# Performance work log

Measured on AMD Instinct MI355X. Metric: run time of the kernel, lower is better.

The kernel has to match this reference:

```python
import jax, jax.numpy as jnp
import numpy as np

T, N, E, DH = 4, 10000, 160000, 256
BN_EPS = 1e-5


def setup_inputs() -> dict:
    key = jax.random.key(0)
    ks = jax.random.split(key, 6)
    node_data = jax.random.normal(ks[0], (T, N, DH), dtype=jnp.float32)
    edge_index = jax.random.randint(ks[1], (2, E), 0, N)
    edge_weight = jax.random.uniform(ks[2], (T, E), dtype=jnp.float32)
    W1 = jax.random.normal(ks[3], (3 * DH, DH), dtype=jnp.float32) * 0.02
    b1 = jnp.zeros((DH,), dtype=jnp.float32)
    gamma = jnp.ones((DH,), dtype=jnp.float32)
    beta = jnp.zeros((DH,), dtype=jnp.float32)
    return {"node_data": node_data, "edge_weight": edge_weight, "W1": W1,
            "b1": b1, "gamma": gamma, "beta": beta, "edge_index": edge_index}


def reference(node_data, edge_weight, W1, b1, gamma, beta, edge_index):
    # edge_index: [2, E] with row 0 = source j, row 1 = destination i
    # (ew[t, i, j] multiplies node j and accumulates into node i, as in bmm)
    src, dst = edge_index[0], edge_index[1]

    # sparse bmm: sum_j ew[t,i,j] * node_data[t,j,:]  -> [T, N, DH]
    weighted = node_data[:, src, :] * edge_weight[..., None]  # [T, E, DH]
    sum_neighbor = jax.vmap(lambda m: jax.ops.segment_sum(m, dst, num_segments=N))(weighted)

    # Z = torch.sparse.sum(ew, dim=2); Z[Z == 0] = 1
    Z = jax.vmap(lambda w: jax.ops.segment_sum(w, dst, num_segments=N))(edge_weight)
    Z = jnp.where(Z == 0, 1.0, Z)[..., None]  # [T, N, 1]
    avg_neighbor = sum_neighbor / Z

    # prev_state = cat([zeros(1,N,dh), node_data[1:]], dim=0)  (as in source)
    prev_state = jnp.concatenate(
        [jnp.zeros((1, N, DH), node_data.dtype), node_data[1:]], axis=0)

    x = jnp.concatenate([node_data, prev_state, avg_neighbor], axis=2)
    x = x.reshape(T * N, 3 * DH)

    # ReluFCN: Linear(3*dh -> dh) -> BatchNorm1d (batch stats) -> ReLU
    h = x @ W1 + b1  # [T*N, DH]
    mean = h.mean(axis=0)
    var = h.var(axis=0)
    h = (h - mean) * jax.lax.rsqrt(var + BN_EPS) * gamma + beta
    h = jax.nn.relu(h)
    return h.reshape(T, N, DH)
```

## Files before the change

### kernel.cpp

```cpp
#include <hip/hip_runtime.h>

enum { TT = 4, NNODES = 10000, NEDGES = 160000 };

typedef short v8s __attribute__((ext_vector_type(8)));
typedef float v4f __attribute__((ext_vector_type(4)));

static __device__ __forceinline__ float bf2f(unsigned short u) {
    union { unsigned int i; float f; } c;
    c.i = ((unsigned int)u) << 16;
    return c.f;
}
static __device__ __forceinline__ unsigned short f2bf(float f) {
    union { float f; unsigned int i; } c;
    c.f = f;
    return (unsigned short)((c.i + 0x7FFFu + ((c.i >> 16) & 1u)) >> 16);
}
static __device__ __forceinline__ float u2f(unsigned int u) {
    union { unsigned int i; float f; } c;
    c.i = u;
    return c.f;
}
static __device__ __forceinline__ void acc8(float* a, float w, uint4 u) {
    a[0] += w * u2f(u.x << 16);
    a[1] += w * u2f(u.x & 0xffff0000u);
    a[2] += w * u2f(u.y << 16);
    a[3] += w * u2f(u.y & 0xffff0000u);
    a[4] += w * u2f(u.z << 16);
    a[5] += w * u2f(u.z & 0xffff0000u);
    a[6] += w * u2f(u.w << 16);
    a[7] += w * u2f(u.w & 0xffff0000u);
}

__global__ void GraphConvLayer_91061896610587_kernel() {}

__global__ void zero_k(int* p, int n) {
    int i = blockIdx.x * 256 + threadIdx.x;
    if (i < n) p[i] = 0;
}

__global__ void prep_k(const unsigned short* ndu, const void* s0, const void* s1,
                       const void* s2, int* mode, float* gammaf, float* betaf) {
    __shared__ int cnt;
    __shared__ int score[6];
    __shared__ float vals[6][256];
    int d = threadIdx.x;
    if (d == 0) cnt = 0;
    if (d < 6) score[d] = 0;
    __syncthreads();
    int c = 0;
    for (int j = 0; j < 16; ++j) {
        unsigned short u = ndu[d * 16 + j];
        if ((u & 0x7FFF) >= 0x6000) ++c;
    }
    if (c) atomicAdd(&cnt, c);
    const void* ptrs[3];
    ptrs[0] = s0; ptrs[1] = s1; ptrs[2] = s2;
    for (int q = 0; q < 6; ++q) {
        const void* p = ptrs[q % 3];
        float v = (q < 3) ? bf2f(((const unsigned short*)p)[d]) : ((const float*)p)[d];
        vals[q][d] = v;
        float av = fabsf(v);
        if (av > 0.25f && av < 4.0f) atomicAdd(&score[q], 1);
    }
    __syncthreads();
    if (d == 0) *mode = (cnt > 0) ? 0 : 1;
    int best = 0;
    for (int q = 1; q < 6; ++q)
        if (score[q] > score[best]) best = q;
    float g = (score[best] > 0) ? vals[best][d] : 1.0f;
    int interp = (best >= 3) ? 3 : 0;
    int bslot  = ((best % 3) == 2) ? 1 : 2;
    float b = vals[interp + bslot][d];
    if (!(b == b) || fabsf(b) > 100.f) b = 0.f;
    gammaf[d] = g;
    betaf[d]  = b;
}

__global__ void canon_nd(const int* mode, const void* nd_raw, unsigned short* ndc) {
    if (*mode != 0) return;
    int i = blockIdx.x * 256 + threadIdx.x;
    float4 v = ((const float4*)nd_raw)[i];
    ushort4 o;
    o.x = f2bf(v.x); o.y = f2bf(v.y); o.z = f2bf(v.z); o.w = f2bf(v.w);
    ((ushort4*)ndc)[i] = o;
}

__global__ void pack_w(const int* mode, const void* W1, float* w2f,
                       short* wp0, short* wp1) {
    int gid = blockIdx.x * 256 + threadIdx.x;
    int v   = gid >> 17;
    int rem = gid & 131071;
    int k   = rem >> 8;
    int n   = rem & 255;
    int m   = *mode;
    const unsigned short* Wb = (const unsigned short*)W1;
    const float*          Wf = (const float*)W1;
    float val;
    if (k < 256) {
        val = m ? bf2f(Wb[k * 256 + n]) : Wf[k * 256 + n];
        if (v) val += m ? bf2f(Wb[(k + 256) * 256 + n]) : Wf[(k + 256) * 256 + n];
    } else {
        val = m ? bf2f(Wb[(k + 256) * 256 + n]) : Wf[(k + 256) * 256 + n];
    }
    if (w2f) w2f[v * 131072 + k * 256 + n] = val;
    if (wp0) {
        int dst = ((k >> 5) * 256 + n) * 32 + (k & 31);
        (v ? wp1 : wp0)[dst] = (short)f2bf(val);
    }
}

__global__ void hist_k(const int* ei, int* counts) {
    int e = blockIdx.x * 256 + threadIdx.x;
    if (e < NEDGES) atomicAdd(&counts[ei[NEDGES + e]], 1);
}

__global__ void scan_k(const int* counts, int* offsets) {
    __shared__ int part[256];
    __shared__ int excl[257];
    int t = threadIdx.x;
    int b = t * 40, e = b + 40;
    if (e > NNODES) e = NNODES;
    int s = 0;
    for (int i = b; i < e; ++i) s += counts[i];
    part[t] = s;
    __syncthreads();
    if (t == 0) {
        int run = 0;
        for (int i = 0; i < 256; ++i) { excl[i] = run; run += part[i]; }
        excl[256] = run;
    }
    __syncthreads();
    int run = excl[t];
    for (int i = b; i < e; ++i) { offsets[i] = run; run += counts[i]; }
    if (t == 0) offsets[NNODES] = excl[256];
}

__global__ void scat_k(const int* ei, const int* offsets, int* cursors,
                       int* ssrc, int* seid) {
    int e = blockIdx.x * 256 + threadIdx.x;
    if (e >= NEDGES) return;
    int d = ei[NEDGES + e];
    int pos = offsets[d] + atomicAdd(&cursors[d], 1);
    ssrc[pos] = ei[e];
    seid[pos] = e;
}

__global__ void wgath_k(const int* mode, const void* ew_raw, const int* seid,
                        float* wcsr) {
    int i = blockIdx.x * 256 + threadIdx.x;
    int t = i / NEDGES, p = i - t * NEDGES;
    int e = seid[p];
    wcsr[i] = (*mode == 1) ? bf2f(((const unsigned short*)ew_raw)[t * NEDGES + e])
                           : ((const float*)ew_raw)[t * NEDGES + e];
}

__global__ __launch_bounds__(256) void fused_k(
    const int* mode, const void* nd_raw, const unsigned short* ndc,
    const float* wcsr, const int* offsets, const int* ssrc,
    const short* wp0, const short* wp1,
    unsigned short* h16, float* colsumB, float* colsumsqB) {
    __shared__ unsigned short xs[32 * 520];
    const unsigned short* ndb = (*mode == 1) ? (const unsigned short*)nd_raw : ndc;
    int t   = blockIdx.y;
    int rb  = blockIdx.x * 32;
    int tid = threadIdx.x;

    int node = tid >> 3;
    int sub  = tid & 7;
    int dq   = sub * 32;
    int du   = sub * 4;
    int growc = min(rb + node, NNODES - 1);
    const uint4* ndg = (const uint4*)(ndb + (size_t)t * NNODES * 256);

    uint4 c0 = ndg[(size_t)growc * 32 + du + 0];
    uint4 c1 = ndg[(size_t)growc * 32 + du + 1];
    uint4 c2 = ndg[(size_t)growc * 32 + du + 2];
    uint4 c3 = ndg[(size_t)growc * 32 + du + 3];
    *(uint4*)&xs[node * 520 + dq]      = c0;
    *(uint4*)&xs[node * 520 + dq + 8]  = c1;
    *(uint4*)&xs[node * 520 + dq + 16] = c2;
    *(uint4*)&xs[node * 520 + dq + 24] = c3;

    float a1[32];
#pragma unroll
    for (int j = 0; j < 32; ++j) a1[j] = 0.f;
    float Z = 0.f;
    const float* wrow = wcsr + t * NEDGES;
    int b = offsets[growc], e = offsets[growc + 1];
    int p = b;
    for (; p + 2 <= e; p += 2) {
        int s0 = ssrc[p], s1 = ssrc[p + 1];
        float w0 = wrow[p], w1 = wrow[p + 1];
        const uint4* r0 = ndg + (size_t)s0 * 32 + du;
        const uint4* r1 = ndg + (size_t)s1 * 32 + du;
        uint4 A0 = r0[0], A1 = r0[1], A2 = r0[2], A3 = r0[3];
        uint4 B0 = r1[0], B1 = r1[1], B2 = r1[2], B3 = r1[3];
        Z += w0 + w1;
        acc8(a1 + 0,  w0, A0); acc8(a1 + 8,  w0, A1);
        acc8(a1 + 16, w0, A2); acc8(a1 + 24, w0, A3);
        acc8(a1 + 0,  w1, B0); acc8(a1 + 8,  w1, B1);
        acc8(a1 + 16, w1, B2); acc8(a1 + 24, w1, B3);
    }
    for (; p < e; ++p) {
        int s = ssrc[p];
        float w = wrow[p];
        const uint4* r0 = ndg + (size_t)s * 32 + du;
        uint4 A0 = r0[0], A1 = r0[1], A2 = r0[2], A3 = r0[3];
        Z += w;
        acc8(a1 + 0,  w, A0); acc8(a1 + 8,  w, A1);
        acc8(a1 + 16, w, A2); acc8(a1 + 24, w, A3);
    }
    float inv = (Z == 0.f) ? 1.f : (1.f / Z);
#pragma unroll
    for (int j = 0; j < 32; j += 4) {
        ushort4 o;
        o.x = f2bf(a1[j] * inv);
        o.y = f2bf(a1[j + 1] * inv);
        o.z = f2bf(a1[j + 2] * inv);
        o.w = f2bf(a1[j + 3] * inv);
        *(ushort4*)&xs[node * 520 + 256 + dq + j] = o;
    }
    __syncthreads();

    int wave = tid >> 6;
    int lane = tid & 63;
    int lane15 = lane & 15, quad = lane >> 4;
    const v8s* wp8 = (const v8s*)(t ? wp1 : wp0);

    v4f acc[2][4];
    v4f zero = {0.f, 0.f, 0.f, 0.f};
#pragma unroll
    for (int mf = 0; mf < 2; ++mf)
#pragma unroll
        for (int nf = 0; nf < 4; ++nf) acc[mf][nf] = zero;

#pragma unroll
    for (int kc = 0; kc < 16; ++kc) {
        v8s a0 = *(const v8s*)&xs[lane15 * 520 + kc * 32 + quad * 8];
        v8s a1v = *(const v8s*)&xs[(lane15 + 16) * 520 + kc * 32 + quad * 8];
#pragma unroll
        for (int nf = 0; nf < 4; ++nf) {
            int ntg = wave * 4 + nf;
            v8s bf = wp8[(size_t)(kc * 256 + ntg * 16 + lane15) * 4 + quad];
            acc[0][nf] = __builtin_amdgcn_mfma_f32_16x16x32_bf16(a0, bf, acc[0][nf], 0, 0, 0);
            acc[1][nf] = __builtin_amdgcn_mfma_f32_16x16x32_bf16(a1v, bf, acc[1][nf], 0, 0, 0);
        }
    }

    int bucket = blockIdx.x & 63;
#pragma unroll
    for (int nf = 0; nf < 4; ++nf) {
        int col = (wave * 4 + nf) * 16 + lane15;
        float s1 = 0.f, s2 = 0.f;
#pragma unroll
        for (int mf = 0; mf < 2; ++mf) {
            int rbase = rb + mf * 16 + quad * 4;
#pragma unroll
            for (int r = 0; r < 4; ++r) {
                int row = rbase + r;
                if (row < NNODES) {
                    float v = acc[mf][nf][r];
                    h16[(size_t)(t * NNODES + row) * 256 + col] = f2bf(v);
                    s1 += v; s2 += v * v;
                }
            }
        }
        s1 += __shfl_xor(s1, 16, 64); s1 += __shfl_xor(s1, 32, 64);
        s2 += __shfl_xor(s2, 16, 64); s2 += __shfl_xor(s2, 32, 64);
        if (quad == 0) {
            atomicAdd(&colsumB[bucket * 256 + col], s1);
            atomicAdd(&colsumsqB[bucket * 256 + col], s2);
        }
    }
}

__global__ void statsB_k(const float* colsumB, const float* colsumsqB,
                         const float* gammaf, const float* betaf,
                         float* scale, float* shiftv) {
    int d = threadIdx.x;
    float s1 = 0.f, s2 = 0.f;
    for (int b = 0; b < 64; ++b) {
        s1 += colsumB[b * 256 + d];
        s2 += colsumsqB[b * 256 + d];
    }
    float mean = s1 * (1.f / 40000.f);
    float var  = s2 * (1.f / 40000.f) - mean * mean;
    if (var < 0.f) var = 0.f;
    if (!(var < 1e30f) || !(mean == mean)) { scale[d] = 0.f; shiftv[d] = 2.5f; return; }
    float r  = rsqrtf(var + 1e-5f);
    float sc = gammaf[d] * r;
    scale[d]  = sc;
    shiftv[d] = betaf[d] - mean * sc;
}

__global__ void normb_k(const unsigned short* h16, const float* scale,
                        const float* shiftv, float* out) {
    int i = blockIdx.x * 256 + threadIdx.x;
    int c0 = (i & 63) * 4;
    ushort4 h = ((const ushort4*)h16)[i];
    float4 o;
    float v;
    v = bf2f(h.x) * scale[c0 + 0] + shiftv[c0 + 0]; if (!(v == v)) v = 1.f; o.x = v > 0.f ? v : 0.f;
    v = bf2f(h.y) * scale[c0 + 1] + shiftv[c0 + 1]; if (!(v == v)) v = 1.f; o.y = v > 0.f ? v : 0.f;
    v = bf2f(h.z) * scale[c0 + 2] + shiftv[c0 + 2]; if (!(v == v)) v = 1.f; o.z = v > 0.f ? v : 0.f;
    v = bf2f(h.w) * scale[c0 + 3] + shiftv[c0 + 3]; if (!(v == v)) v = 1.f; o.w = v > 0.f ? v : 0.f;
    ((float4*)out)[i] = o;
}

__global__ void aggv_k(const int* mode, const void* nd_raw, const void* ew_raw,
                       const int* offsets, const int* ssrc, const int* seid,
                       unsigned short* avg) {
    int m   = *mode;
    int wid = blockIdx.x * 4 + (threadIdx.x >> 6);
    int t = wid / NNODES, n = wid - t * NNODES;
    int lane = threadIdx.x & 63;
    float a0 = 0.f, a1 = 0.f, a2 = 0.f, a3 = 0.f, Z = 0.f;
    int b = offsets[n], e = offsets[n + 1];
    for (int p = b; p < e; ++p) {
        int s = ssrc[p];
        int ewi = t * NEDGES + seid[p];
        float w = m ? bf2f(((const unsigned short*)ew_raw)[ewi])
                    : ((const float*)ew_raw)[ewi];
        Z += w;
        int vidx = (t * NNODES + s) * 64 + lane;
        if (m) {
            ushort4 v = ((const ushort4*)nd_raw)[vidx];
            a0 += w * bf2f(v.x); a1 += w * bf2f(v.y);
            a2 += w * bf2f(v.z); a3 += w * bf2f(v.w);
        } else {
            float4 v = ((const float4*)nd_raw)[vidx];
            a0 += w * v.x; a1 += w * v.y; a2 += w * v.z; a3 += w * v.w;
        }
    }
    float inv = (Z == 0.f) ? 1.f : (1.f / Z);
    ushort4 o;
    o.x = f2bf(a0 * inv); o.y = f2bf(a1 * inv);
    o.z = f2bf(a2 * inv); o.w = f2bf(a3 * inv);
    ((ushort4*)avg)[(t * NNODES + n) * 64 + lane] = o;
}

__global__ __launch_bounds__(256) void gemmv_k(
    const int* mode, const void* nd_raw, const unsigned short* avg,
    const float* w2f, float* hbuf) {
    __shared__ float xsf[16 * 512];
    int m   = *mode;
    int bt  = blockIdx.x / 625;
    int rb0 = (blockIdx.x - bt * 625) * 16;
    int tid = threadIdx.x;
    for (int j = 0; j < 32; ++j) {
        int idx = tid + j * 256;
        int r = idx >> 9, k = idx & 511;
        int grow = (bt * NNODES + rb0 + r) * 256;
        float val;
        if (k < 256)
            val = m ? bf2f(((const unsigned short*)nd_raw)[grow + k])
                    : ((const float*)nd_raw)[grow + k];
        else
            val = bf2f(avg[grow + (k - 256)]);
        xsf[idx] = val;
    }
    __syncthreads();
    int r0 = (tid >> 6) * 4;
    const float4* w4 = (const float4*)(w2f + (bt ? 131072 : 0));
    float acc[4][4];
#pragma unroll
    for (int r = 0; r < 4; ++r)
#pragma unroll
        for (int c = 0; c < 4; ++c) acc[r][c] = 0.f;
    const float* x0 = &xsf[(r0 + 0) * 512];
    const float* x1 = &xsf[(r0 + 1) * 512];
    const float* x2 = &xsf[(r0 + 2) * 512];
    const float* x3 = &xsf[(r0 + 3) * 512];
#pragma unroll 8
    for (int k = 0; k < 512; ++k) {
        float4 wv = w4[k * 64 + (tid & 63)];
        float a = x0[k], b = x1[k], c = x2[k], d = x3[k];
        acc[0][0] += a * wv.x; acc[0][1] += a * wv.y; acc[0][2] += a * wv.z; acc[0][3] += a * wv.w;
        acc[1][0] += b * wv.x; acc[1][1] += b * wv.y; acc[1][2] += b * wv.z; acc[1][3] += b * wv.w;
        acc[2][0] += c * wv.x; acc[2][1] += c * wv.y; acc[2][2] += c * wv.z; acc[2][3] += c * wv.w;
        acc[3][0] += d * wv.x; acc[3][1] += d * wv.y; acc[3][2] += d * wv.z; acc[3][3] += d * wv.w;
    }
#pragma unroll
    for (int r = 0; r < 4; ++r) {
        int grow = bt * NNODES + rb0 + r0 + r;
        float4 o;
        o.x = acc[r][0]; o.y = acc[r][1]; o.z = acc[r][2]; o.w = acc[r][3];
        ((float4*)hbuf)[grow * 64 + (tid & 63)] = o;
    }
}

__global__ void stats2_k(const float* hbuf, float* colsum, float* colsumsq) {
    int col = threadIdx.x;
    int rb  = blockIdx.x * 250;
    float s1 = 0.f, s2 = 0.f;
    for (int j = 0; j < 250; ++j) {
        float v = hbuf[(size_t)(rb + j) * 256 + col];
        s1 += v; s2 += v * v;
    }
    atomicAdd(&colsum[col], s1);
    atomicAdd(&colsumsq[col], s2);
}

__global__ void stats_k(const float* colsum, const float* colsumsq,
                        const float* gammaf, const float* betaf,
                        float* scale, float* shiftv) {
    int d = threadIdx.x;
    float mean = colsum[d] * (1.f / 40000.f);
    float var  = colsumsq[d] * (1.f / 40000.f) - mean * mean;
    if (var < 0.f) var = 0.f;
    if (!(var < 1e30f) || !(mean == mean)) { scale[d] = 0.f; shiftv[d] = 2.5f; return; }
    float r  = rsqrtf(var + 1e-5f);
    float sc = gammaf[d] * r;
    scale[d]  = sc;
    shiftv[d] = betaf[d] - mean * sc;
}

__global__ void norm_k(float* hbuf, const float* scale, const float* shiftv) {
    int i = blockIdx.x * 256 + threadIdx.x;
    int c0 = (i & 63) * 4;
    float4 h = ((const float4*)hbuf)[i];
    float4 o;
    float v;
    v = h.x * scale[c0 + 0] + shiftv[c0 + 0]; if (!(v == v)) v = 1.f; o.x = v > 0.f ? v : 0.f;
    v = h.y * scale[c0 + 1] + shiftv[c0 + 1]; if (!(v == v)) v = 1.f; o.y = v > 0.f ? v : 0.f;
    v = h.z * scale[c0 + 2] + shiftv[c0 + 2]; if (!(v == v)) v = 1.f; o.z = v > 0.f ? v : 0.f;
    v = h.w * scale[c0 + 3] + shiftv[c0 + 3]; if (!(v == v)) v = 1.f; o.w = v > 0.f ? v : 0.f;
    ((float4*)hbuf)[i] = o;
}

extern "C" void kernel_launch(void* const* d_in, const int* in_sizes, int n_in,
                              void* d_out, int out_size, void* d_ws, size_t ws_size,
                              hipStream_t stream) {
    const void* nd = d_in[0];
    const void* ew = d_in[1];
    const void* W1 = d_in[2];
    const void* p3 = d_in[3];
    const void* p4 = d_in[4];
    const void* p5 = d_in[5];
    const void* ei = d_in[6];
    {
        const void *nd_ = 0, *ew_ = 0, *W1_ = 0, *ei_ = 0, *s_[3] = {0, 0, 0};
        int ns = 0;
        for (int i = 0; i < n_in; ++i) {
            int s = in_sizes[i];
            if      (s == 10240000) nd_ = d_in[i];
            else if (s == 640000)   ew_ = d_in[i];
            else if (s == 196608)   W1_ = d_in[i];
            else if (s == 320000)   ei_ = d_in[i];
            else if (s == 256 && ns < 3) s_[ns++] = d_in[i];
        }
        if (nd_ && ew_ && W1_ && ei_ && ns == 3) {
            nd = nd_; ew = ew_; W1 = W1_; ei = ei_;
            p3 = s_[0]; p4 = s_[1]; p5 = s_[2];
        }
    }
    float* outp = (float*)d_out;
    const unsigned short* ndu = (const unsigned short*)nd;
    const int* eii = (const int*)ei;

    char* ws = (char*)d_ws;

    if (ws_size >= (size_t)45582464) {
        int*   counts    = (int*)(ws + 0);
        int*   cursors   = (int*)(ws + 40960);
        int*   mode      = (int*)(ws + 81920);
        float* scale     = (float*)(ws + 82944);
        float* shiftv    = (float*)(ws + 83968);
        float* gammaf    = (float*)(ws + 84992);
        float* betaf     = (float*)(ws + 86016);
        float* colsumB   = (float*)(ws + 87040);
        float* colsumsqB = (float*)(ws + 152576);
        int*   offsets   = (int*)(ws + 218112);
        int*   ssrc      = (int*)(ws + 258176);
        int*   seid      = (int*)(ws + 898176);
        float* wcsr      = (float*)(ws + 1538176);
        short* wp0       = (short*)(ws + 4098176);
        short* wp1       = (short*)(ws + 4360320);
        unsigned short* ndc = (unsigned short*)(ws + 4622464);
        unsigned short* h16 = (unsigned short*)(ws + 25102464);
        float* noW = 0;

        zero_k<<<213, 256, 0, stream>>>((int*)ws, 54528);
        prep_k<<<1, 256, 0, stream>>>(ndu, p3, p4, p5, mode, gammaf, betaf);
        canon_nd<<<10000, 256, 0, stream>>>(mode, nd, ndc);
        pack_w<<<1024, 256, 0, stream>>>(mode, W1, noW, wp0, wp1);
        hist_k<<<625, 256, 0, stream>>>(eii, counts);
        scan_k<<<1, 256, 0, stream>>>(counts, offsets);
        scat_k<<<625, 256, 0, stream>>>(eii, offsets, cursors, ssrc, seid);
        wgath_k<<<2500, 256, 0, stream>>>(mode, ew, seid, wcsr);
        fused_k<<<dim3(313, 4), 256, 0, stream>>>(mode, nd, ndc, wcsr, offsets, ssrc,
                                                  wp0, wp1, h16, colsumB, colsumsqB);
        statsB_k<<<1, 256, 0, stream>>>(colsumB, colsumsqB, gammaf, betaf, scale, shiftv);
        normb_k<<<10000, 256, 0, stream>>>(h16, scale, shiftv, outp);
    } else {
        int*   counts   = (int*)(ws + 0);
        int*   cursors  = (int*)(ws + 40960);
        float* colsum   = (float*)(ws + 81920);
        float* colsumsq = (float*)(ws + 82944);
        int*   mode     = (int*)(ws + 83968);
        float* scale    = (float*)(ws + 84032);
        float* shiftv   = (float*)(ws + 85056);
        float* gammaf   = (float*)(ws + 86080);
        float* betaf    = (float*)(ws + 87104);
        int*   offsets  = (int*)(ws + 88128);
        int*   ssrc     = (int*)(ws + 128192);
        int*   seid     = (int*)(ws + 768192);
        float* w2f      = (float*)(ws + 1408192);
        unsigned short* avg = (unsigned short*)(ws + 2457600);
        short* nowp = 0;

        zero_k<<<83, 256, 0, stream>>>((int*)ws, 20994);
        prep_k<<<1, 256, 0, stream>>>(ndu, p3, p4, p5, mode, gammaf, betaf);
        pack_w<<<1024, 256, 0, stream>>>(mode, W1, w2f, nowp, nowp);
        hist_k<<<625, 256, 0, stream>>>(eii, counts);
        scan_k<<<1, 256, 0, stream>>>(counts, offsets);
        scat_k<<<625, 256, 0, stream>>>(eii, offsets, cursors, ssrc, seid);
        aggv_k<<<10000, 256, 0, stream>>>(mode, nd, ew, offsets, ssrc, seid, avg);
        gemmv_k<<<2500, 256, 0, stream>>>(mode, nd, avg, w2f, outp);
        stats2_k<<<160, 256, 0, stream>>>(outp, colsum, colsumsq);
        stats_k<<<1, 256, 0, stream>>>(colsum, colsumsq, gammaf, betaf, scale, shiftv);
        norm_k<<<10000, 256, 0, stream>>>(outp, scale, shiftv);
    }
}
```

Measured before the change: 254.6 us.

## Merge prep kernels, remap fused blocks across XCDs, coalesce gathers, use nontemporal I/O

The zeroing and prep kernels become one launch. Bf16 conversion of node data, weight packing and the edge histogram become another. The CSR scatter now also gathers edge weights, which removes the separate wgath pass. Together this cuts the launch count and an extra pass over seid. fused_k switches to a 1D grid that maps each timestep to XCD-aligned block ids for L2 locality. Its per-thread row loads are interleaved (sub, sub+8, ...) so neighbouring lanes read contiguous 16-byte chunks. The h16 write, its read in normb_k and the output store use nontemporal hints, which could hurt if h16 would otherwise stay resident in cache.

```diff
diff --git a/kernel.cpp b/kernel.cpp
--- a/kernel.cpp
+++ b/kernel.cpp
@@ -4,6 +4,7 @@
 
 typedef short v8s __attribute__((ext_vector_type(8)));
 typedef float v4f __attribute__((ext_vector_type(4)));
+typedef unsigned short u16x4 __attribute__((ext_vector_type(4)));
 
 static __device__ __forceinline__ float bf2f(unsigned short u) {
     union { unsigned int i; float f; } c;
@@ -76,13 +77,83 @@
     betaf[d]  = b;
 }
 
-__global__ void canon_nd(const int* mode, const void* nd_raw, unsigned short* ndc) {
-    if (*mode != 0) return;
-    int i = blockIdx.x * 256 + threadIdx.x;
-    float4 v = ((const float4*)nd_raw)[i];
-    ushort4 o;
-    o.x = f2bf(v.x); o.y = f2bf(v.y); o.z = f2bf(v.z); o.w = f2bf(v.w);
-    ((ushort4*)ndc)[i] = o;
+__global__ void zp_k(int* zp, int zn, const unsigned short* ndu, const void* s0,
+                     const void* s1, const void* s2, int* mode, float* gammaf,
+                     float* betaf) {
+    __shared__ int cnt;
+    __shared__ int score[6];
+    __shared__ float vals[6][256];
+    if (blockIdx.x < 213) {
+        int i = blockIdx.x * 256 + threadIdx.x;
+        if (i < zn) zp[i] = 0;
+        return;
+    }
+    int d = threadIdx.x;
+    if (d == 0) cnt = 0;
+    if (d < 6) score[d] = 0;
+    __syncthreads();
+    int c = 0;
+    for (int j = 0; j < 16; ++j) {
+        unsigned short u = ndu[d * 16 + j];
+        if ((u & 0x7FFF) >= 0x6000) ++c;
+    }
+    if (c) atomicAdd(&cnt, c);
+    const void* ptrs[3];
+    ptrs[0] = s0; ptrs[1] = s1; ptrs[2] = s2;
+    for (int q = 0; q < 6; ++q) {
+        const void* p = ptrs[q % 3];
+        float v = (q < 3) ? bf2f(((const unsigned short*)p)[d]) : ((const float*)p)[d];
+        vals[q][d] = v;
+        float av = fabsf(v);
+        if (av > 0.25f && av < 4.0f) atomicAdd(&score[q], 1);
+    }
+    __syncthreads();
+    if (d == 0) *mode = (cnt > 0) ? 0 : 1;
+    int best = 0;
+    for (int q = 1; q < 6; ++q)
+        if (score[q] > score[best]) best = q;
+    float g = (score[best] > 0) ? vals[best][d] : 1.0f;
+    int interp = (best >= 3) ? 3 : 0;
+    int bslot  = ((best % 3) == 2) ? 1 : 2;
+    float b = vals[interp + bslot][d];
+    if (!(b == b) || fabsf(b) > 100.f) b = 0.f;
+    gammaf[d] = g;
+    betaf[d]  = b;
+}
+
+__global__ void cph_k(const int* mode, const void* nd_raw, unsigned short* ndc,
+                      const void* W1, short* wp0, short* wp1,
+                      const int* ei, int* counts) {
+    int bb = blockIdx.x;
+    if (bb < 10000) {
+        if (*mode != 0) return;
+        int i = bb * 256 + threadIdx.x;
+        float4 v = ((const float4*)nd_raw)[i];
+        ushort4 o;
+        o.x = f2bf(v.x); o.y = f2bf(v.y); o.z = f2bf(v.z); o.w = f2bf(v.w);
+        ((ushort4*)ndc)[i] = o;
+    } else if (bb < 11024) {
+        int gid = (bb - 10000) * 256 + threadIdx.x;
+        int v   = gid >> 17;
+        int rem = gid & 131071;
+        int k   = rem >> 8;
+        int n   = rem & 255;
+        int m   = *mode;
+        const unsigned short* Wb = (const unsigned short*)W1;
+        const float*          Wf = (const float*)W1;
+        float val;
+        if (k < 256) {
+            val = m ? bf2f(Wb[k * 256 + n]) : Wf[k * 256 + n];
+            if (v) val += m ? bf2f(Wb[(k + 256) * 256 + n]) : Wf[(k + 256) * 256 + n];
+        } else {
+            val = m ? bf2f(Wb[(k + 256) * 256 + n]) : Wf[(k + 256) * 256 + n];
+        }
+        int dst = ((k >> 5) * 256 + n) * 32 + (k & 31);
+        (v ? wp1 : wp0)[dst] = (short)f2bf(val);
+    } else {
+        int e = (bb - 11024) * 256 + threadIdx.x;
+        if (e < NEDGES) atomicAdd(&counts[ei[NEDGES + e]], 1);
+    }
 }
 
 __global__ void pack_w(const int* mode, const void* W1, float* w2f,
@@ -145,13 +216,22 @@
     seid[pos] = e;
 }
 
-__global__ void wgath_k(const int* mode, const void* ew_raw, const int* seid,
+__global__ void scatw_k(const int* mode, const int* ei, const void* ew_raw,
+                        const int* offsets, int* cursors, int* ssrc, int* seid,
                         float* wcsr) {
-    int i = blockIdx.x * 256 + threadIdx.x;
-    int t = i / NEDGES, p = i - t * NEDGES;
-    int e = seid[p];
-    wcsr[i] = (*mode == 1) ? bf2f(((const unsigned short*)ew_raw)[t * NEDGES + e])
-                           : ((const float*)ew_raw)[t * NEDGES + e];
+    int e = blockIdx.x * 256 + threadIdx.x;
+    if (e >= NEDGES) return;
+    int d = ei[NEDGES + e];
+    int pos = offsets[d] + atomicAdd(&cursors[d], 1);
+    ssrc[pos] = ei[e];
+    seid[pos] = e;
+    int m = *mode;
+#pragma unroll
+    for (int t = 0; t < TT; ++t) {
+        float w = m ? bf2f(((const unsigned short*)ew_raw)[t * NEDGES + e])
+                    : ((const float*)ew_raw)[t * NEDGES + e];
+        wcsr[t * NEDGES + pos] = w;
+    }
 }
 
 __global__ __launch_bounds__(256) void fused_k(
@@ -160,26 +240,29 @@
     const short* wp0, const short* wp1,
     unsigned short* h16, float* colsumB, float* colsumsqB) {
     __shared__ unsigned short xs[32 * 520];
+    int id  = blockIdx.x;
+    int xcd = id & 7;
+    int t   = xcd & 3;
+    int rbi = ((id >> 3) << 1) + (xcd >> 2);
+    if (rbi >= 313) return;
+    int rb  = rbi * 32;
     const unsigned short* ndb = (*mode == 1) ? (const unsigned short*)nd_raw : ndc;
-    int t   = blockIdx.y;
-    int rb  = blockIdx.x * 32;
     int tid = threadIdx.x;
 
     int node = tid >> 3;
     int sub  = tid & 7;
-    int dq   = sub * 32;
-    int du   = sub * 4;
     int growc = min(rb + node, NNODES - 1);
     const uint4* ndg = (const uint4*)(ndb + (size_t)t * NNODES * 256);
-
-    uint4 c0 = ndg[(size_t)growc * 32 + du + 0];
-    uint4 c1 = ndg[(size_t)growc * 32 + du + 1];
-    uint4 c2 = ndg[(size_t)growc * 32 + du + 2];
-    uint4 c3 = ndg[(size_t)growc * 32 + du + 3];
-    *(uint4*)&xs[node * 520 + dq]      = c0;
-    *(uint4*)&xs[node * 520 + dq + 8]  = c1;
-    *(uint4*)&xs[node * 520 + dq + 16] = c2;
-    *(uint4*)&xs[node * 520 + dq + 24] = c3;
+    const uint4* own = ndg + (size_t)growc * 32;
+
+    uint4 c0 = own[sub];
+    uint4 c1 = own[sub + 8];
+    uint4 c2 = own[sub + 16];
+    uint4 c3 = own[sub + 24];
+    *(uint4*)&xs[node * 520 + sub * 8]            = c0;
+    *(uint4*)&xs[node * 520 + (sub + 8) * 8]      = c1;
+    *(uint4*)&xs[node * 520 + (sub + 16) * 8]     = c2;
+    *(uint4*)&xs[node * 520 + (sub + 24) * 8]     = c3;
 
     float a1[32];
 #pragma unroll
@@ -191,10 +274,10 @@
     for (; p + 2 <= e; p += 2) {
         int s0 = ssrc[p], s1 = ssrc[p + 1];
         float w0 = wrow[p], w1 = wrow[p + 1];
-        const uint4* r0 = ndg + (size_t)s0 * 32 + du;
-        const uint4* r1 = ndg + (size_t)s1 * 32 + du;
-        uint4 A0 = r0[0], A1 = r0[1], A2 = r0[2], A3 = r0[3];
-        uint4 B0 = r1[0], B1 = r1[1], B2 = r1[2], B3 = r1[3];
+        const uint4* r0 = ndg + (size_t)s0 * 32;
+        const uint4* r1 = ndg + (size_t)s1 * 32;
+        uint4 A0 = r0[sub], A1 = r0[sub + 8], A2 = r0[sub + 16], A3 = r0[sub + 24];
+        uint4 B0 = r1[sub], B1 = r1[sub + 8], B2 = r1[sub + 16], B3 = r1[sub + 24];
         Z += w0 + w1;
         acc8(a1 + 0,  w0, A0); acc8(a1 + 8,  w0, A1);
         acc8(a1 + 16, w0, A2); acc8(a1 + 24, w0, A3);
@@ -204,21 +287,26 @@
     for (; p < e; ++p) {
         int s = ssrc[p];
         float w = wrow[p];
-        const uint4* r0 = ndg + (size_t)s * 32 + du;
-        uint4 A0 = r0[0], A1 = r0[1], A2 = r0[2], A3 = r0[3];
+        const uint4* r0 = ndg + (size_t)s * 32;
+        uint4 A0 = r0[sub], A1 = r0[sub + 8], A2 = r0[sub + 16], A3 = r0[sub + 24];
         Z += w;
         acc8(a1 + 0,  w, A0); acc8(a1 + 8,  w, A1);
         acc8(a1 + 16, w, A2); acc8(a1 + 24, w, A3);
     }
     float inv = (Z == 0.f) ? 1.f : (1.f / Z);
 #pragma unroll
-    for (int j = 0; j < 32; j += 4) {
-        ushort4 o;
-        o.x = f2bf(a1[j] * inv);
-        o.y = f2bf(a1[j + 1] * inv);
-        o.z = f2bf(a1[j + 2] * inv);
-        o.w = f2bf(a1[j + 3] * inv);
-        *(ushort4*)&xs[node * 520 + 256 + dq + j] = o;
+    for (int j = 0; j < 4; ++j) {
+        ushort4 lo, hi;
+        lo.x = f2bf(a1[j * 8 + 0] * inv);
+        lo.y = f2bf(a1[j * 8 + 1] * inv);
+        lo.z = f2bf(a1[j * 8 + 2] * inv);
+        lo.w = f2bf(a1[j * 8 + 3] * inv);
+        hi.x = f2bf(a1[j * 8 + 4] * inv);
+        hi.y = f2bf(a1[j * 8 + 5] * inv);
+        hi.z = f2bf(a1[j * 8 + 6] * inv);
+        hi.w = f2bf(a1[j * 8 + 7] * inv);
+        *(ushort4*)&xs[node * 520 + 256 + (sub + 8 * j) * 8]     = lo;
+        *(ushort4*)&xs[node * 520 + 256 + (sub + 8 * j) * 8 + 4] = hi;
     }
     __syncthreads();
 
@@ -247,7 +335,7 @@
         }
     }
 
-    int bucket = blockIdx.x & 63;
+    int bucket = id & 63;
 #pragma unroll
     for (int nf = 0; nf < 4; ++nf) {
         int col = (wave * 4 + nf) * 16 + lane15;
@@ -260,7 +348,8 @@
                 int row = rbase + r;
                 if (row < NNODES) {
                     float v = acc[mf][nf][r];
-                    h16[(size_t)(t * NNODES + row) * 256 + col] = f2bf(v);
+                    __builtin_nontemporal_store(
+                        f2bf(v), &h16[(size_t)(t * NNODES + row) * 256 + col]);
                     s1 += v; s2 += v * v;
                 }
             }
@@ -297,14 +386,14 @@
                         const float* shiftv, float* out) {
     int i = blockIdx.x * 256 + threadIdx.x;
     int c0 = (i & 63) * 4;
-    ushort4 h = ((const ushort4*)h16)[i];
-    float4 o;
+    u16x4 h = __builtin_nontemporal_load(&((const u16x4*)h16)[i]);
+    v4f o;
     float v;
     v = bf2f(h.x) * scale[c0 + 0] + shiftv[c0 + 0]; if (!(v == v)) v = 1.f; o.x = v > 0.f ? v : 0.f;
     v = bf2f(h.y) * scale[c0 + 1] + shiftv[c0 + 1]; if (!(v == v)) v = 1.f; o.y = v > 0.f ? v : 0.f;
     v = bf2f(h.z) * scale[c0 + 2] + shiftv[c0 + 2]; if (!(v == v)) v = 1.f; o.z = v > 0.f ? v : 0.f;
     v = bf2f(h.w) * scale[c0 + 3] + shiftv[c0 + 3]; if (!(v == v)) v = 1.f; o.w = v > 0.f ? v : 0.f;
-    ((float4*)out)[i] = o;
+    __builtin_nontemporal_store(o, &((v4f*)out)[i]);
 }
 
 __global__ void aggv_k(const int* mode, const void* nd_raw, const void* ew_raw,
@@ -478,18 +567,15 @@
         short* wp1       = (short*)(ws + 4360320);
         unsigned short* ndc = (unsigned short*)(ws + 4622464);
         unsigned short* h16 = (unsigned short*)(ws + 25102464);
-        float* noW = 0;
-
-        zero_k<<<213, 256, 0, stream>>>((int*)ws, 54528);
-        prep_k<<<1, 256, 0, stream>>>(ndu, p3, p4, p5, mode, gammaf, betaf);
-        canon_nd<<<10000, 256, 0, stream>>>(mode, nd, ndc);
-        pack_w<<<1024, 256, 0, stream>>>(mode, W1, noW, wp0, wp1);
-        hist_k<<<625, 256, 0, stream>>>(eii, counts);
+
+        zp_k<<<214, 256, 0, stream>>>((int*)ws, 54528, ndu, p3, p4, p5,
+                                      mode, gammaf, betaf);
+        cph_k<<<11649, 256, 0, stream>>>(mode, nd, ndc, W1, wp0, wp1, eii, counts);
         scan_k<<<1, 256, 0, stream>>>(counts, offsets);
-        scat_k<<<625, 256, 0, stream>>>(eii, offsets, cursors, ssrc, seid);
-        wgath_k<<<2500, 256, 0, stream>>>(mode, ew, seid, wcsr);
-        fused_k<<<dim3(313, 4), 256, 0, stream>>>(mode, nd, ndc, wcsr, offsets, ssrc,
-                                                  wp0, wp1, h16, colsumB, colsumsqB);
+        scatw_k<<<625, 256, 0, stream>>>(mode, eii, ew, offsets, cursors,
+                                         ssrc, seid, wcsr);
+        fused_k<<<1280, 256, 0, stream>>>(mode, nd, ndc, wcsr, offsets, ssrc,
+                                          wp0, wp1, h16, colsumB, colsumsqB);
         statsB_k<<<1, 256, 0, stream>>>(colsumB, colsumsqB, gammaf, betaf, scale, shiftv);
         normb_k<<<10000, 256, 0, stream>>>(h16, scale, shiftv, outp);
     } else {
```

After: 233.0 us. 1.09x faster.
